# Performance work log

Hardware: AMD Instinct MI355X
Metric: run time of the kernel (lower is better)

## Reference

```python
import jax, jax.numpy as jnp
import numpy as np

DIM = 1024
NUM_HEADS = 16
HEAD_DIM = DIM // NUM_HEADS
SCALE = HEAD_DIM ** -0.5


def setup_inputs() -> dict:
    key = jax.random.key(0)
    ks = jax.random.split(key, 11)
    B, T = 2, 2048
    std = DIM ** -0.5
    return {
        "query": jax.random.normal(ks[0], (B, T, DIM), jnp.float32),
        "key": jax.random.normal(ks[1], (B, T, DIM), jnp.float32),
        "value": jax.random.normal(ks[2], (B, T, DIM), jnp.float32),
        "wq": jax.random.normal(ks[3], (DIM, DIM), jnp.float32) * std,
        "bq": jnp.zeros((DIM,), jnp.float32),
        "wk": jax.random.normal(ks[4], (DIM, DIM), jnp.float32) * std,
        "bk": jnp.zeros((DIM,), jnp.float32),
        "wv": jax.random.normal(ks[5], (DIM, DIM), jnp.float32) * std,
        "bv": jnp.zeros((DIM,), jnp.float32),
        "wo": jax.random.normal(ks[6], (DIM, DIM), jnp.float32) * std,
        "bo": jnp.zeros((DIM,), jnp.float32),
    }


def reference(query, key, value, wq, bq, wk, bk, wv, bv, wo, bo):
    B, Tq, D = query.shape
    Tk = key.shape[1]
    H, Hd = NUM_HEADS, HEAD_DIM
    # projections (torch Linear: x @ W^T + b); reshape to [B, H, T, Hd]
    q = (query @ wq.T + bq).reshape(B, Tq, H, Hd).transpose(0, 2, 1, 3)
    k = (key @ wk.T + bk).reshape(B, Tk, H, Hd).transpose(0, 2, 1, 3)
    v = (value @ wv.T + bv).reshape(B, Tk, H, Hd).transpose(0, 2, 1, 3)
    # attention scores [B, H, Tq, Tk]
    attn = jnp.einsum("bhqd,bhkd->bhqk", q, k) * SCALE
    attn = jax.nn.softmax(attn, axis=-1)
    # dropout p=0.0 -> identity
    out = jnp.einsum("bhqk,bhkd->bhqd", attn, v)
    out = out.transpose(0, 2, 1, 3).reshape(B, Tq, D)
    return out @ wo.T + bo
```

## Files before the change

### kernel.cpp

```cpp
#include <hip/hip_runtime.h>
#include <math.h>


typedef __attribute__((ext_vector_type(8))) short short8;
typedef __attribute__((ext_vector_type(4))) float f32x4;
typedef __attribute__((ext_vector_type(4))) float float4v;
typedef __attribute__((ext_vector_type(4))) unsigned short ushort4v;
typedef __attribute__((ext_vector_type(2))) unsigned int uint2v;

typedef __attribute__((address_space(3))) unsigned int lds_uint;
typedef __attribute__((address_space(1))) unsigned int glb_uint;

__device__ __forceinline__ void gload_lds16(const void* g, void* l) {
    __builtin_amdgcn_global_load_lds((glb_uint*)(unsigned long long)g,
                                     (lds_uint*)(unsigned int)(unsigned long long)l,
                                     16, 0, 0);
}

__device__ __forceinline__ unsigned short f32_bf16(float f) {
    union { float f; unsigned int u; } x; x.f = f;
    unsigned int r = x.u + 0x7fffu + ((x.u >> 16) & 1u);
    return (unsigned short)(r >> 16);
}

__device__ __forceinline__ unsigned int cvt_pk_bf16(float lo, float hi) {
    unsigned int r;
    asm("v_cvt_pk_bf16_f32 %0, %1, %2" : "=v"(r) : "v"(lo), "v"(hi));
    return r;
}

__device__ __forceinline__ float exp2_fast(float x) {
    float r;
    asm("v_exp_f32 %0, %1" : "=v"(r) : "v"(x));
    return r;
}

#define QSCALE 0.18033688011112042f

__global__ void pack3_bf16(const float* __restrict__ a, const float* __restrict__ b,
                           const float* __restrict__ c,
                           unsigned short* __restrict__ oa, unsigned short* __restrict__ ob,
                           unsigned short* __restrict__ oc, int n4) {
    const int y = blockIdx.y;
    const float* in = (y == 0) ? a : (y == 1) ? b : c;
    unsigned short* out = (y == 0) ? oa : (y == 1) ? ob : oc;
    int i = blockIdx.x * blockDim.x + threadIdx.x;
    if (i < n4) {
        float4v v = ((const float4v*)in)[i];
        ushort4v o;
        o.x = f32_bf16(v.x); o.y = f32_bf16(v.y);
        o.z = f32_bf16(v.z); o.w = f32_bf16(v.w);
        ((ushort4v*)out)[i] = o;
    }
}

__global__ void pack4_bf16(const float* __restrict__ a, const float* __restrict__ b,
                           const float* __restrict__ c, const float* __restrict__ d,
                           unsigned short* __restrict__ oa, unsigned short* __restrict__ ob,
                           unsigned short* __restrict__ oc, unsigned short* __restrict__ od,
                           int n4) {
    const int y = blockIdx.y;
    const float* in = (y == 0) ? a : (y == 1) ? b : (y == 2) ? c : d;
    unsigned short* out = (y == 0) ? oa : (y == 1) ? ob : (y == 2) ? oc : od;
    int i = blockIdx.x * blockDim.x + threadIdx.x;
    if (i < n4) {
        float4v v = ((const float4v*)in)[i];
        ushort4v o;
        o.x = f32_bf16(v.x); o.y = f32_bf16(v.y);
        o.z = f32_bf16(v.z); o.w = f32_bf16(v.w);
        ((ushort4v*)out)[i] = o;
    }
}

__global__ __launch_bounds__(256, 2) void gemm_qkv(
    const unsigned short* __restrict__ A0, const unsigned short* __restrict__ A1,
    const unsigned short* __restrict__ A2,
    const unsigned short* __restrict__ W0, const unsigned short* __restrict__ W1,
    const unsigned short* __restrict__ W2,
    const float* __restrict__ bs0, const float* __restrict__ bs1,
    const float* __restrict__ bs2,
    unsigned short* __restrict__ O0, unsigned short* __restrict__ O1,
    unsigned short* __restrict__ O2)
{
    const int z = blockIdx.z;
    const unsigned short* A = (z == 0) ? A0 : (z == 1) ? A1 : A2;
    const unsigned short* W = (z == 0) ? W0 : (z == 1) ? W1 : W2;
    const float* bias        = (z == 0) ? bs0 : (z == 1) ? bs1 : bs2;
    unsigned short* C        = (z == 0) ? O0 : (z == 1) ? O1 : O2;
    const float oscale = (z == 0) ? QSCALE : 1.0f;
    const int N = 1024, K = 1024;

    __shared__ unsigned short As[128 * 64];
    __shared__ unsigned short Bs[128 * 64];
    const int tid  = threadIdx.x;
    const int lane = tid & 63, wave = tid >> 6;
    const int l15 = lane & 15, l4 = lane >> 4;
    const int bm = blockIdx.y * 128, bn = blockIdx.x * 128;
    const int wr = wave >> 1, wc = wave & 1;
    const int swz = l15 & 7;

    f32x4 acc[4][4];
    #pragma unroll
    for (int i = 0; i < 4; ++i)
        #pragma unroll
        for (int j = 0; j < 4; ++j)
            #pragma unroll
            for (int e = 0; e < 4; ++e) acc[i][j][e] = 0.f;

    const int srow = lane >> 3;
    const int scol = ((lane & 7) ^ srow) * 8;

    for (int k0 = 0; k0 < K; k0 += 64) {
        __syncthreads();
        #pragma unroll
        for (int i = 0; i < 4; ++i) {
            int c = wave * 4 + i;
            int row = c * 8 + srow;
            gload_lds16(A + (size_t)(bm + row) * K + k0 + scol, &As[c * 512]);
            gload_lds16(W + (size_t)(bn + row) * K + k0 + scol, &Bs[c * 512]);
        }
        __syncthreads();
        #pragma unroll
        for (int kk = 0; kk < 2; ++kk) {
            short8 af[4], bf[4];
            const int ko = ((kk * 4 + l4) ^ swz) << 3;
            #pragma unroll
            for (int i = 0; i < 4; ++i)
                af[i] = *(const short8*)&As[(wr * 64 + i * 16 + l15) * 64 + ko];
            #pragma unroll
            for (int j = 0; j < 4; ++j)
                bf[j] = *(const short8*)&Bs[(wc * 64 + j * 16 + l15) * 64 + ko];
            #pragma unroll
            for (int i = 0; i < 4; ++i)
                #pragma unroll
                for (int j = 0; j < 4; ++j)
                    acc[i][j] = __builtin_amdgcn_mfma_f32_16x16x32_bf16(
                        af[i], bf[j], acc[i][j], 0, 0, 0);
        }
    }

    #pragma unroll
    for (int j = 0; j < 4; ++j) {
        const int col = bn + wc * 64 + j * 16 + l15;
        const float bj = bias[col];
        #pragma unroll
        for (int i = 0; i < 4; ++i) {
            const int row0 = bm + wr * 64 + i * 16 + l4 * 4;
            #pragma unroll
            for (int r = 0; r < 4; ++r) {
                const int row = row0 + r;
                const float v = (acc[i][j][r] + bj) * oscale;
                if (z < 2) {
                    C[(size_t)row * N + col] = f32_bf16(v);
                } else {
                    const int b = row >> 11, t = row & 2047;
                    C[(((size_t)((b << 4) + (col >> 6)) * 64
                        + (col & 63)) << 11) + t] = f32_bf16(v);
                }
            }
        }
    }
}

__global__ __launch_bounds__(256, 3) void gemm_out(
    const unsigned short* __restrict__ A,
    const unsigned short* __restrict__ W,
    const float* __restrict__ bias,
    float* __restrict__ C)
{
    const int N = 1024, K = 1024;
    __shared__ unsigned short As[2][64 * 64];
    __shared__ unsigned short Bs[2][128 * 64];
    const int tid  = threadIdx.x;
    const int lane = tid & 63, wave = tid >> 6;
    const int l15 = lane & 15, l4 = lane >> 4;
    const int bm = blockIdx.y * 64, bn = blockIdx.x * 128;
    const int wr = wave >> 1, wc = wave & 1;
    const int swz = l15 & 7;

    f32x4 acc[2][4];
    #pragma unroll
    for (int i = 0; i < 2; ++i)
        #pragma unroll
        for (int j = 0; j < 4; ++j)
            #pragma unroll
            for (int e = 0; e < 4; ++e) acc[i][j][e] = 0.f;

    const int srow = lane >> 3;
    const int scol = ((lane & 7) ^ srow) * 8;

    auto stage = [&](int bf, int k0) {
        #pragma unroll
        for (int i = 0; i < 2; ++i) {
            const int c = wave * 2 + i;
            gload_lds16(A + (size_t)(bm + c * 8 + srow) * K + k0 + scol,
                        &As[bf][c * 512]);
        }
        #pragma unroll
        for (int i = 0; i < 4; ++i) {
            const int c = wave * 4 + i;
            gload_lds16(W + (size_t)(bn + c * 8 + srow) * K + k0 + scol,
                        &Bs[bf][c * 512]);
        }
    };

    stage(0, 0);
    __syncthreads();

    int bufi = 0;
    for (int k0 = 0; k0 < K; k0 += 64) {
        if (k0 + 64 < K) stage(bufi ^ 1, k0 + 64);
        #pragma unroll
        for (int kk = 0; kk < 2; ++kk) {
            short8 af[2], bf[4];
            const int ko = ((kk * 4 + l4) ^ swz) << 3;
            #pragma unroll
            for (int i = 0; i < 2; ++i)
                af[i] = *(const short8*)&As[bufi][(wr * 32 + i * 16 + l15) * 64 + ko];
            #pragma unroll
            for (int j = 0; j < 4; ++j)
                bf[j] = *(const short8*)&Bs[bufi][(wc * 64 + j * 16 + l15) * 64 + ko];
            #pragma unroll
            for (int i = 0; i < 2; ++i)
                #pragma unroll
                for (int j = 0; j < 4; ++j)
                    acc[i][j] = __builtin_amdgcn_mfma_f32_16x16x32_bf16(
                        af[i], bf[j], acc[i][j], 0, 0, 0);
        }
        __syncthreads();
        bufi ^= 1;
    }

    #pragma unroll
    for (int j = 0; j < 4; ++j) {
        const int col = bn + wc * 64 + j * 16 + l15;
        const float bj = bias[col];
        #pragma unroll
        for (int i = 0; i < 2; ++i) {
            const int row0 = bm + wr * 32 + i * 16 + l4 * 4;
            #pragma unroll
            for (int r = 0; r < 4; ++r)
                C[(size_t)(row0 + r) * N + col] = acc[i][j][r] + bj;
        }
    }
}

__global__ __launch_bounds__(512, 4) void attn_fwd(
    const unsigned short* __restrict__ qp,
    const unsigned short* __restrict__ kp,
    const unsigned short* __restrict__ vt,
    unsigned short* __restrict__ op)
{
    __shared__ unsigned short Ks[2][128 * 64];
    __shared__ unsigned short Vs[2][2][64 * 64];
    __shared__ unsigned short P[8][16 * 64];

    const int tid = threadIdx.x;
    const int lane = tid & 63, wave = tid >> 6;
    const int l15 = lane & 15, l4 = lane >> 4;
    const int swz = (l15 & 7) << 3;

    const int flat = blockIdx.x;
    const int swzb = (flat & 7) * 64 + (flat >> 3);
    const int bx = swzb & 15;
    const int bh = swzb >> 4;
    const int b = bh >> 4, h = bh & 15;
    const int q0 = bx * 128 + wave * 16;

    const size_t xbase = (size_t)b * 2048 * 1024 + h * 64;
    const size_t vbase = (size_t)bh * 64 * 2048;

    const int sr = lane >> 3;
    const int sc = ((lane & 7) ^ sr) * 8;

    short8 bq[2];
    #pragma unroll
    for (int kk = 0; kk < 2; ++kk)
        bq[kk] = *(const short8*)&qp[xbase
            + (size_t)(q0 + l15) * 1024 + kk * 32 + l4 * 8];

    f32x4 acc[4];
    #pragma unroll
    for (int dj = 0; dj < 4; ++dj)
        #pragma unroll
        for (int e = 0; e < 4; ++e) acc[dj][e] = 0.f;

    float m_run = -1e30f, l_part = 0.f;

    auto stage = [&](int bf, int kv0) {
        #pragma unroll
        for (int i = 0; i < 2; ++i) {
            const int c = wave * 2 + i;
            gload_lds16(kp + xbase + (size_t)(kv0 + c * 8 + sr) * 1024 + sc,
                        &Ks[bf][c * 512]);
        }
        #pragma unroll
        for (int h2 = 0; h2 < 2; ++h2)
            gload_lds16(vt + vbase + (size_t)(wave * 8 + sr) * 2048
                            + kv0 + h2 * 64 + sc,
                        &Vs[bf][h2][wave * 512]);
    };

    stage(0, 0);
    __syncthreads();

    const int NT = 2048 / 128;
    int buf = 0;
    for (int t = 0; t < NT; ++t) {
        if (t + 1 < NT) stage(buf ^ 1, (t + 1) * 128);

        #pragma unroll
        for (int hh = 0; hh < 2; ++hh) {
            f32x4 st[4];
            {
                short8 ak[4];
                #pragma unroll
                for (int j = 0; j < 4; ++j)
                    ak[j] = *(const short8*)&Ks[buf][(hh * 64 + j * 16 + l15) * 64
                                                     + ((l4 << 3) ^ swz)];
                const f32x4 z4 = {0.f, 0.f, 0.f, 0.f};
                #pragma unroll
                for (int j = 0; j < 4; ++j)
                    st[j] = __builtin_amdgcn_mfma_f32_16x16x32_bf16(
                        ak[j], bq[0], z4, 0, 0, 0);
                #pragma unroll
                for (int j = 0; j < 4; ++j)
                    ak[j] = *(const short8*)&Ks[buf][(hh * 64 + j * 16 + l15) * 64
                                                     + (((4 + l4) << 3) ^ swz)];
                #pragma unroll
                for (int j = 0; j < 4; ++j)
                    st[j] = __builtin_amdgcn_mfma_f32_16x16x32_bf16(
                        ak[j], bq[1], st[j], 0, 0, 0);
            }

            short8 av[2][4];
            #pragma unroll
            for (int kvc = 0; kvc < 2; ++kvc)
                #pragma unroll
                for (int dj = 0; dj < 4; ++dj)
                    av[kvc][dj] = *(const short8*)&Vs[buf][hh]
                        [(dj * 16 + l15) * 64 + (((kvc * 4 + l4) << 3) ^ swz)];

            {
                float tm[4];
                #pragma unroll
                for (int j = 0; j < 4; ++j)
                    tm[j] = fmaxf(fmaxf(st[j][0], st[j][1]),
                                  fmaxf(st[j][2], st[j][3]));
                float mx = fmaxf(fmaxf(tm[0], tm[1]), fmaxf(tm[2], tm[3]));
                mx = fmaxf(mx, __shfl_xor(mx, 16));
                mx = fmaxf(mx, __shfl_xor(mx, 32));
                if (!__all(mx - m_run <= 8.0f)) {
                    const float mnew = fmaxf(m_run, mx);
                    const float corr = exp2_fast(m_run - mnew);
                    m_run = mnew;
                    l_part *= corr;
                    #pragma unroll
                    for (int dj = 0; dj < 4; ++dj) acc[dj] *= corr;
                }
                float ts[4];
                #pragma unroll
                for (int j = 0; j < 4; ++j) {
                    float p0 = exp2_fast(st[j][0] - m_run);
                    float p1 = exp2_fast(st[j][1] - m_run);
                    float p2 = exp2_fast(st[j][2] - m_run);
                    float p3 = exp2_fast(st[j][3] - m_run);
                    st[j][0] = p0; st[j][1] = p1;
                    st[j][2] = p2; st[j][3] = p3;
                    ts[j] = (p0 + p1) + (p2 + p3);
                }
                l_part += (ts[0] + ts[1]) + (ts[2] + ts[3]);
            }

            #pragma unroll
            for (int j = 0; j < 4; ++j) {
                uint2v w;
                w.x = cvt_pk_bf16(st[j][0], st[j][1]);
                w.y = cvt_pk_bf16(st[j][2], st[j][3]);
                *(uint2v*)&P[wave][l15 * 64 + ((j * 16 + l4 * 4) ^ swz)] = w;
            }

            #pragma unroll
            for (int kvc = 0; kvc < 2; ++kvc) {
                short8 pb = *(const short8*)&P[wave][l15 * 64
                                                + (((kvc * 4 + l4) << 3) ^ swz)];
                #pragma unroll
                for (int dj = 0; dj < 4; ++dj)
                    acc[dj] = __builtin_amdgcn_mfma_f32_16x16x32_bf16(
                        av[kvc][dj], pb, acc[dj], 0, 0, 0);
            }
        }

        __syncthreads();
        buf ^= 1;
    }

    {
        float l = l_part;
        l += __shfl_xor(l, 16);
        l += __shfl_xor(l, 32);
        const float inv = 1.0f / l;
        const int t = q0 + l15;
        #pragma unroll
        for (int dj = 0; dj < 4; ++dj) {
            uint2v w;
            w.x = cvt_pk_bf16(acc[dj][0] * inv, acc[dj][1] * inv);
            w.y = cvt_pk_bf16(acc[dj][2] * inv, acc[dj][3] * inv);
            *(uint2v*)&op[((size_t)(b * 2048 + t)) * 1024
                          + h * 64 + dj * 16 + l4 * 4] = w;
        }
    }
}

extern "C" void kernel_launch(void* const* d_in, const int* in_sizes, int n_in,
                              void* d_out, int out_size, void* d_ws, size_t ws_size,
                              hipStream_t stream)
{
    const float* q  = (const float*)d_in[0];
    const float* k  = (const float*)d_in[1];
    const float* v  = (const float*)d_in[2];
    const float* wq = (const float*)d_in[3];
    const float* bq = (const float*)d_in[4];
    const float* wk = (const float*)d_in[5];
    const float* bk = (const float*)d_in[6];
    const float* wv = (const float*)d_in[7];
    const float* bv = (const float*)d_in[8];
    const float* wo = (const float*)d_in[9];
    const float* bo = (const float*)d_in[10];
    float* out = (float*)d_out;

    const int M = 4096, N = 1024, K = 1024;
    unsigned char* ws = (unsigned char*)d_ws;
    const size_t SX = (size_t)M * K * 2;
    const size_t SW = (size_t)N * K * 2;
    unsigned short* xq  = (unsigned short*)(ws);
    unsigned short* xk  = (unsigned short*)(ws + SX);
    unsigned short* xv  = (unsigned short*)(ws + 2 * SX);
    unsigned short* wqb = (unsigned short*)(ws + 3 * SX);
    unsigned short* wkb = (unsigned short*)(ws + 3 * SX + SW);
    unsigned short* wvb = (unsigned short*)(ws + 3 * SX + 2 * SW);
    unsigned short* wob = (unsigned short*)(ws + 3 * SX + 3 * SW);
    unsigned short* qp  = (unsigned short*)(ws + 3 * SX + 4 * SW);
    unsigned short* kp  = qp + (size_t)M * N;
    unsigned short* vt  = kp + (size_t)M * N;
    unsigned short* opb = vt + (size_t)M * N;

    pack3_bf16<<<dim3(4096, 3), 256, 0, stream>>>(q, k, v, xq, xk, xv,
                                                  M * K / 4);
    pack4_bf16<<<dim3(1024, 4), 256, 0, stream>>>(wq, wk, wv, wo,
                                                  wqb, wkb, wvb, wob, N * K / 4);

    gemm_qkv<<<dim3(8, 32, 3), 256, 0, stream>>>(xq, xk, xv, wqb, wkb, wvb,
                                                 bq, bk, bv, qp, kp, vt);

    attn_fwd<<<dim3(512), 512, 0, stream>>>(qp, kp, vt, opb);

    gemm_out<<<dim3(8, 64), 256, 0, stream>>>(opb, wob, bo, out);
}
```

Measured before the change: 128.7 us.

## Double-buffer QKV GEMM with 64-row tiles and defer softmax max reduction

The QKV projection GEMM now uses a 64x128 tile with double-buffered LDS staging, so the next K-slice is loaded while the current one feeds MFMA. The grid doubles and launch bounds allow three blocks per CU, adding parallelism and latency hiding at the cost of less A/B reuse per tile. In attention, the cross-lane shuffle reduction of the row max is skipped unless some lane's local max exceeds the running max by the threshold, which removes shuffles from the common path.

```diff
diff --git a/kernel.cpp b/kernel.cpp
--- a/kernel.cpp
+++ b/kernel.cpp
@@ -72,7 +72,7 @@
     }
 }
 
-__global__ __launch_bounds__(256, 2) void gemm_qkv(
+__global__ __launch_bounds__(256, 3) void gemm_qkv(
     const unsigned short* __restrict__ A0, const unsigned short* __restrict__ A1,
     const unsigned short* __restrict__ A2,
     const unsigned short* __restrict__ W0, const unsigned short* __restrict__ W1,
@@ -90,18 +90,18 @@
     const float oscale = (z == 0) ? QSCALE : 1.0f;
     const int N = 1024, K = 1024;
 
-    __shared__ unsigned short As[128 * 64];
-    __shared__ unsigned short Bs[128 * 64];
+    __shared__ unsigned short As[2][64 * 64];
+    __shared__ unsigned short Bs[2][128 * 64];
     const int tid  = threadIdx.x;
     const int lane = tid & 63, wave = tid >> 6;
     const int l15 = lane & 15, l4 = lane >> 4;
-    const int bm = blockIdx.y * 128, bn = blockIdx.x * 128;
+    const int bm = blockIdx.y * 64, bn = blockIdx.x * 128;
     const int wr = wave >> 1, wc = wave & 1;
     const int swz = l15 & 7;
 
-    f32x4 acc[4][4];
-    #pragma unroll
-    for (int i = 0; i < 4; ++i)
+    f32x4 acc[2][4];
+    #pragma unroll
+    for (int i = 0; i < 2; ++i)
         #pragma unroll
         for (int j = 0; j < 4; ++j)
             #pragma unroll
@@ -110,33 +110,46 @@
     const int srow = lane >> 3;
     const int scol = ((lane & 7) ^ srow) * 8;
 
+    auto stage = [&](int bf, int k0) {
+        #pragma unroll
+        for (int i = 0; i < 2; ++i) {
+            const int c = wave * 2 + i;
+            gload_lds16(A + (size_t)(bm + c * 8 + srow) * K + k0 + scol,
+                        &As[bf][c * 512]);
+        }
+        #pragma unroll
+        for (int i = 0; i < 4; ++i) {
+            const int c = wave * 4 + i;
+            gload_lds16(W + (size_t)(bn + c * 8 + srow) * K + k0 + scol,
+                        &Bs[bf][c * 512]);
+        }
+    };
+
+    stage(0, 0);
+    __syncthreads();
+
+    int bufi = 0;
     for (int k0 = 0; k0 < K; k0 += 64) {
-        __syncthreads();
-        #pragma unroll
-        for (int i = 0; i < 4; ++i) {
-            int c = wave * 4 + i;
-            int row = c * 8 + srow;
-            gload_lds16(A + (size_t)(bm + row) * K + k0 + scol, &As[c * 512]);
-            gload_lds16(W + (size_t)(bn + row) * K + k0 + scol, &Bs[c * 512]);
-        }
-        __syncthreads();
+        if (k0 + 64 < K) stage(bufi ^ 1, k0 + 64);
         #pragma unroll
         for (int kk = 0; kk < 2; ++kk) {
-            short8 af[4], bf[4];
+            short8 af[2], bf[4];
             const int ko = ((kk * 4 + l4) ^ swz) << 3;
             #pragma unroll
-            for (int i = 0; i < 4; ++i)
-                af[i] = *(const short8*)&As[(wr * 64 + i * 16 + l15) * 64 + ko];
+            for (int i = 0; i < 2; ++i)
+                af[i] = *(const short8*)&As[bufi][(wr * 32 + i * 16 + l15) * 64 + ko];
             #pragma unroll
             for (int j = 0; j < 4; ++j)
-                bf[j] = *(const short8*)&Bs[(wc * 64 + j * 16 + l15) * 64 + ko];
-            #pragma unroll
-            for (int i = 0; i < 4; ++i)
+                bf[j] = *(const short8*)&Bs[bufi][(wc * 64 + j * 16 + l15) * 64 + ko];
+            #pragma unroll
+            for (int i = 0; i < 2; ++i)
                 #pragma unroll
                 for (int j = 0; j < 4; ++j)
                     acc[i][j] = __builtin_amdgcn_mfma_f32_16x16x32_bf16(
                         af[i], bf[j], acc[i][j], 0, 0, 0);
         }
+        __syncthreads();
+        bufi ^= 1;
     }
 
     #pragma unroll
@@ -144,8 +157,8 @@
         const int col = bn + wc * 64 + j * 16 + l15;
         const float bj = bias[col];
         #pragma unroll
-        for (int i = 0; i < 4; ++i) {
-            const int row0 = bm + wr * 64 + i * 16 + l4 * 4;
+        for (int i = 0; i < 2; ++i) {
+            const int row0 = bm + wr * 32 + i * 16 + l4 * 4;
             #pragma unroll
             for (int r = 0; r < 4; ++r) {
                 const int row = row0 + r;
@@ -347,10 +360,11 @@
                 for (int j = 0; j < 4; ++j)
                     tm[j] = fmaxf(fmaxf(st[j][0], st[j][1]),
                                   fmaxf(st[j][2], st[j][3]));
-                float mx = fmaxf(fmaxf(tm[0], tm[1]), fmaxf(tm[2], tm[3]));
-                mx = fmaxf(mx, __shfl_xor(mx, 16));
-                mx = fmaxf(mx, __shfl_xor(mx, 32));
-                if (!__all(mx - m_run <= 8.0f)) {
+                const float mxl = fmaxf(fmaxf(tm[0], tm[1]),
+                                        fmaxf(tm[2], tm[3]));
+                if (!__all(mxl - m_run <= 8.0f)) {
+                    float mx = fmaxf(mxl, __shfl_xor(mxl, 16));
+                    mx = fmaxf(mx, __shfl_xor(mx, 32));
                     const float mnew = fmaxf(m_run, mx);
                     const float corr = exp2_fast(m_run - mnew);
                     m_run = mnew;
@@ -450,7 +464,7 @@
     pack4_bf16<<<dim3(1024, 4), 256, 0, stream>>>(wq, wk, wv, wo,
                                                   wqb, wkb, wvb, wob, N * K / 4);
 
-    gemm_qkv<<<dim3(8, 32, 3), 256, 0, stream>>>(xq, xk, xv, wqb, wkb, wvb,
+    gemm_qkv<<<dim3(8, 64, 3), 256, 0, stream>>>(xq, xk, xv, wqb, wkb, wvb,
                                                  bq, bk, bv, qp, kp, vt);
 
     attn_fwd<<<dim3(512), 512, 0, stream>>>(qp, kp, vt, opb);
```

Result: no change. 128.2 us (-0.4%).
